# Kernel optimization log

Measured on AMD Instinct MI355X. Metric: run time of the kernel, lower is better.

## Reference

```python
import jax, jax.numpy as jnp
import numpy as np

N, C, D, H, W = 1, 32, 64, 192, 160


def affine_grid_3d(theta, size):
    # PyTorch F.affine_grid 3D, align_corners=True convention.
    n, c, d, h, w = size
    z = jnp.linspace(-1.0, 1.0, d)
    y = jnp.linspace(-1.0, 1.0, h)
    x = jnp.linspace(-1.0, 1.0, w)
    zz, yy, xx = jnp.meshgrid(z, y, x, indexing='ij')          # [D,H,W]
    base = jnp.stack([xx, yy, zz, jnp.ones_like(xx)], axis=-1)  # [D,H,W,4]
    return jnp.einsum('dhwk,nck->ndhwc', base, theta)           # [N,D,H,W,3] (x,y,z)


def _gather_corner(vol, zi, yi, xi):
    # vol: [C,D,H,W]; zi/yi/xi: [D,H,W] int32. Zero padding outside.
    c, d, h, w = vol.shape
    valid = (zi >= 0) & (zi < d) & (yi >= 0) & (yi < h) & (xi >= 0) & (xi < w)
    zc = jnp.clip(zi, 0, d - 1)
    yc = jnp.clip(yi, 0, h - 1)
    xc = jnp.clip(xi, 0, w - 1)
    flat = vol.reshape(c, d * h * w)
    idx = (zc * h + yc) * w + xc
    vals = jnp.take(flat, idx.reshape(-1), axis=1).reshape(c, *zi.shape)
    return vals * valid[None].astype(vol.dtype)


def grid_sample_3d(inp, grid):
    # Trilinear grid_sample, zeros padding, align_corners=True.
    n, c, d, h, w = inp.shape
    x = (grid[..., 0] + 1.0) * 0.5 * (w - 1)
    y = (grid[..., 1] + 1.0) * 0.5 * (h - 1)
    z = (grid[..., 2] + 1.0) * 0.5 * (d - 1)
    x0 = jnp.floor(x).astype(jnp.int32); x1 = x0 + 1
    y0 = jnp.floor(y).astype(jnp.int32); y1 = y0 + 1
    z0 = jnp.floor(z).astype(jnp.int32); z1 = z0 + 1
    wx = (x - x0.astype(x.dtype))
    wy = (y - y0.astype(y.dtype))
    wz = (z - z0.astype(z.dtype))

    def sample_one(vol, z0, z1, y0, y1, x0, x1, wz, wy, wx):
        out = jnp.zeros((vol.shape[0],) + wz.shape, dtype=vol.dtype)
        for zi, wzc in ((z0, 1.0 - wz), (z1, wz)):
            for yi, wyc in ((y0, 1.0 - wy), (y1, wy)):
                for xi, wxc in ((x0, 1.0 - wx), (x1, wx)):
                    out = out + _gather_corner(vol, zi, yi, xi) * (wzc * wyc * wxc)[None]
        return out

    return jax.vmap(sample_one)(inp, z0, z1, y0, y1, x0, x1, wz, wy, wx)


def setup_inputs() -> dict:
    key = jax.random.key(0)
    k1, k2 = jax.random.split(key)
    inp = jax.random.normal(k1, (N, C, D, H, W), dtype=jnp.float32)
    identity = jnp.asarray([1, 0, 0, 0, 0, 1, 0, 0, 0, 0, 1, 0], dtype=jnp.float32)
    theta = identity + 0.1 * jax.random.normal(k2, (12,), dtype=jnp.float32)
    return {"input": inp, "theta": theta}


def reference(input, theta):
    th = theta.reshape(1, 3, 4)
    grid = affine_grid_3d(th, input.shape)       # [N,D,H,W,3]
    out = grid_sample_3d(input, grid)            # [N,C,D,H,W]
    return jnp.transpose(out, (0, 4, 3, 1, 2))   # [N,W,H,C,D]
```

## Files before the change

### kernel.cpp

```cpp
#include <hip/hip_runtime.h>

constexpr int W_ = 160;
constexpr int H_ = 192;
constexpr int D_ = 64;
constexpr int C_ = 32;
constexpr int HW_  = H_ * W_;
constexpr int DHWi = D_ * HW_;
constexpr int CD   = C_ * D_;

constexpr int TW = 32, TH = 12, TD = 16;
constexpr int NWT = W_ / TW;
constexpr int NHT = H_ / TH;
constexpr int NDT = D_ / TD;
constexpr int QPP = NWT * NHT;
constexpr int CPX = C_ / 8;
constexpr int NPH = CPX * NDT;

typedef float f4_t __attribute__((ext_vector_type(4)));
typedef float f2_t __attribute__((ext_vector_type(2)));

__global__ void __launch_bounds__(256, 4)
affine_grid_sample_kernel(const float* __restrict__ inp,
                          const float* __restrict__ th,
                          float* __restrict__ out)
{
    const int t   = threadIdx.x;
    const int bid = blockIdx.x;
    const int xcd = bid & 7;
    int r = bid >> 3;
    const int phase = r / QPP;
    const int q     = r - phase * QPP;
    const int c  = xcd * CPX + (phase >> 2);
    const int dt = phase & 3;
    const int hs = q / NWT;
    const int wt = q - hs * NWT;
    const int w0 = wt * TW, h0 = hs * TH, d0 = dt * TD;

    const float th0=th[0], th1=th[1], th2 =th[2],  th3 =th[3];
    const float th4=th[4], th5=th[5], th6 =th[6],  th7 =th[7];
    const float th8=th[8], th9=th[9], th10=th[10], th11=th[11];

    const float* __restrict__ pc = inp + (size_t)c * DHWi;

    const int wl = t & 15;
    const int dq = (t >> 4) & 3;
    const int wh = (t >> 6) & 1;
    const int hp = t >> 7;
    const int w  = w0 + wh * 16 + wl;
    const float xx = fmaf((float)w, 2.0f / (W_ - 1), -1.0f);

    float kzx[4], kzy[4], kzz[4];
    #pragma unroll
    for (int k = 0; k < 4; ++k) {
        const int d = d0 + 4 * dq + k;
        const float zz = fmaf((float)d, 2.0f / (D_ - 1), -1.0f);
        kzx[k] = fmaf(th2,  zz, th3);
        kzy[k] = fmaf(th6,  zz, th7);
        kzz[k] = fmaf(th10, zz, th11);
    }

    float* const ob = out + ((size_t)w * H_ + h0) * CD + (size_t)c * D_ + d0 + 4 * dq;

    #pragma unroll 1
    for (int hh = hp; hh < TH; hh += 2) {
        const float yy = fmaf((float)(h0 + hh), 2.0f / (H_ - 1), -1.0f);

        unsigned off[4][4];
        float wA[4], wB[4], v0a[4], v1a[4], s0a[4], s1a[4];
        #pragma unroll
        for (int k = 0; k < 4; ++k) {
            const float px = (fmaf(th0, xx, fmaf(th1, yy, kzx[k])) + 1.0f) * (0.5f * (W_ - 1));
            const float py = (fmaf(th4, xx, fmaf(th5, yy, kzy[k])) + 1.0f) * (0.5f * (H_ - 1));
            const float pz = (fmaf(th8, xx, fmaf(th9, yy, kzz[k])) + 1.0f) * (0.5f * (D_ - 1));
            const float fx = floorf(px), fy = floorf(py), fz = floorf(pz);
            const int ix0 = (int)fx, iy0 = (int)fy, iz0 = (int)fz;
            const float wx = px - fx, wy = py - fy, wz = pz - fz;
            const float u0r = ((unsigned)ix0       < (unsigned)W_) ? (1.0f - wx) : 0.0f;
            const float u1r = ((unsigned)(ix0 + 1) < (unsigned)W_) ? wx          : 0.0f;
            v0a[k] = ((unsigned)iy0       < (unsigned)H_) ? (1.0f - wy) : 0.0f;
            v1a[k] = ((unsigned)(iy0 + 1) < (unsigned)H_) ? wy          : 0.0f;
            s0a[k] = ((unsigned)iz0       < (unsigned)D_) ? (1.0f - wz) : 0.0f;
            s1a[k] = ((unsigned)(iz0 + 1) < (unsigned)D_) ? wz          : 0.0f;
            float a = u0r, b = u1r;
            if (ix0 == -1)     { a = u1r; b = 0.0f; }
            if (ix0 == W_ - 1) { a = 0.0f; b = u0r; }
            wA[k] = a; wB[k] = b;
            const int e = min(max(ix0, 0), W_ - 2);
            const int cy0 = min(max(iy0,     0), H_ - 1);
            const int cy1 = min(max(iy0 + 1, 0), H_ - 1);
            const int cz0 = min(max(iz0,     0), D_ - 1);
            const int cz1 = min(max(iz0 + 1, 0), D_ - 1);
            off[k][0] = (unsigned)(cz0 * HW_ + cy0 * W_ + e);
            off[k][1] = (unsigned)(cz0 * HW_ + cy1 * W_ + e);
            off[k][2] = (unsigned)(cz1 * HW_ + cy0 * W_ + e);
            off[k][3] = (unsigned)(cz1 * HW_ + cy1 * W_ + e);
        }

        f2_t P[4][4];
        #pragma unroll
        for (int k = 0; k < 4; ++k)
            #pragma unroll
            for (int j = 0; j < 4; ++j)
                __builtin_memcpy(&P[k][j], pc + off[k][j], 8);

        asm volatile("" ::
            "v"(P[0][0]), "v"(P[0][1]), "v"(P[0][2]), "v"(P[0][3]),
            "v"(P[1][0]), "v"(P[1][1]), "v"(P[1][2]), "v"(P[1][3]),
            "v"(P[2][0]), "v"(P[2][1]), "v"(P[2][2]), "v"(P[2][3]),
            "v"(P[3][0]), "v"(P[3][1]), "v"(P[3][2]), "v"(P[3][3]));
        __builtin_amdgcn_sched_barrier(0);

        f4_t val;
        #pragma unroll
        for (int k = 0; k < 4; ++k) {
            const float x00 = wA[k] * P[k][0][0] + wB[k] * P[k][0][1];
            const float x01 = wA[k] * P[k][1][0] + wB[k] * P[k][1][1];
            const float x10 = wA[k] * P[k][2][0] + wB[k] * P[k][2][1];
            const float x11 = wA[k] * P[k][3][0] + wB[k] * P[k][3][1];
            const float e0 = v0a[k] * x00 + v1a[k] * x01;
            const float e1 = v0a[k] * x10 + v1a[k] * x11;
            val[k] = s0a[k] * e0 + s1a[k] * e1;
        }
        __builtin_nontemporal_store(val, (f4_t*)(ob + (size_t)hh * CD));
    }
}

extern "C" void kernel_launch(void* const* d_in, const int* in_sizes, int n_in,
                              void* d_out, int out_size, void* d_ws, size_t ws_size,
                              hipStream_t stream)
{
    const float* inp = (const float*)d_in[0];
    const float* th  = (const float*)d_in[1];
    float* out = (float*)d_out;

    hipLaunchKernelGGL(affine_grid_sample_kernel, dim3(8 * NPH * QPP), dim3(256),
                       0, stream, inp, th, out);
}
```

Baseline: 644.0 us.

## Stage sampled source bounding box in LDS before trilinear interpolation

```diff
diff --git a/kernel.cpp b/kernel.cpp
--- a/kernel.cpp
+++ b/kernel.cpp
@@ -8,13 +8,14 @@
 constexpr int DHWi = D_ * HW_;
 constexpr int CD   = C_ * D_;
 
-constexpr int TW = 32, TH = 12, TD = 16;
+constexpr int TW = 32, THh = 8, TDt = 4;
 constexpr int NWT = W_ / TW;
-constexpr int NHT = H_ / TH;
-constexpr int NDT = D_ / TD;
+constexpr int NHT = H_ / THh;
+constexpr int NDT = D_ / TDt;
 constexpr int QPP = NWT * NHT;
 constexpr int CPX = C_ / 8;
-constexpr int NPH = CPX * NDT;
+constexpr int BX = 44, BY = 24, BZ = 9;
+constexpr int TOT = BX * BY * BZ;
 
 typedef float f4_t __attribute__((ext_vector_type(4)));
 typedef float f2_t __attribute__((ext_vector_type(2)));
@@ -24,17 +25,19 @@
                           const float* __restrict__ th,
                           float* __restrict__ out)
 {
+    __shared__ float Lb[TOT];
+
     const int t   = threadIdx.x;
     const int bid = blockIdx.x;
     const int xcd = bid & 7;
-    int r = bid >> 3;
-    const int phase = r / QPP;
-    const int q     = r - phase * QPP;
-    const int c  = xcd * CPX + (phase >> 2);
-    const int dt = phase & 3;
-    const int hs = q / NWT;
-    const int wt = q - hs * NWT;
-    const int w0 = wt * TW, h0 = hs * TH, d0 = dt * TD;
+    const int r   = bid >> 3;
+    const int q   = r % QPP;
+    const int rem = r / QPP;
+    const int c   = xcd * CPX + (rem >> 4);
+    const int dt  = rem & 15;
+    const int hs  = q / NWT;
+    const int wt  = q - hs * NWT;
+    const int w0 = wt * TW, h0 = hs * THh, d0 = dt * TDt;
 
     const float th0=th[0], th1=th[1], th2 =th[2],  th3 =th[3];
     const float th4=th[4], th5=th[5], th6 =th[6],  th7 =th[7];
@@ -42,75 +45,179 @@
 
     const float* __restrict__ pc = inp + (size_t)c * DHWi;
 
-    const int wl = t & 15;
-    const int dq = (t >> 4) & 3;
-    const int wh = (t >> 6) & 1;
-    const int hp = t >> 7;
-    const int w  = w0 + wh * 16 + wl;
+    const int wl = t & 31;
+    const int hl = t >> 5;
+    const int w  = w0 + wl;
+    const int h  = h0 + hl;
     const float xx = fmaf((float)w, 2.0f / (W_ - 1), -1.0f);
-
-    float kzx[4], kzy[4], kzz[4];
+    const float yy = fmaf((float)h, 2.0f / (H_ - 1), -1.0f);
+
+    float pxmn= 1e30f, pxmx=-1e30f, pymn= 1e30f, pymx=-1e30f,
+          pzmn= 1e30f, pzmx=-1e30f;
+    #pragma unroll
+    for (int ci = 0; ci < 8; ++ci) {
+        const int cw = (ci & 1) ? w0 + TW  - 1 : w0;
+        const int chh= (ci & 2) ? h0 + THh - 1 : h0;
+        const int cd = (ci & 4) ? d0 + TDt - 1 : d0;
+        const float zzc = fmaf((float)cd, 2.0f / (D_ - 1), -1.0f);
+        const float kxc = fmaf(th2,  zzc, th3);
+        const float kyc = fmaf(th6,  zzc, th7);
+        const float kzc = fmaf(th10, zzc, th11);
+        const float xxc = fmaf((float)cw,  2.0f / (W_ - 1), -1.0f);
+        const float yyc = fmaf((float)chh, 2.0f / (H_ - 1), -1.0f);
+        const float px = (fmaf(th0, xxc, fmaf(th1, yyc, kxc)) + 1.0f) * (0.5f * (W_ - 1));
+        const float py = (fmaf(th4, xxc, fmaf(th5, yyc, kyc)) + 1.0f) * (0.5f * (H_ - 1));
+        const float pz = (fmaf(th8, xxc, fmaf(th9, yyc, kzc)) + 1.0f) * (0.5f * (D_ - 1));
+        pxmn = fminf(pxmn, px); pxmx = fmaxf(pxmx, px);
+        pymn = fminf(pymn, py); pymx = fmaxf(pymx, py);
+        pzmn = fminf(pzmn, pz); pzmx = fmaxf(pzmx, pz);
+    }
+    const int xlo = max((int)floorf(pxmn), 0);
+    const int xhi = min((int)floorf(pxmx) + 1, W_ - 1);
+    const int ylo = max((int)floorf(pymn), 0);
+    const int yhi = min((int)floorf(pymx) + 1, H_ - 1);
+    const int zlo = max((int)floorf(pzmn), 0);
+    const int zhi = min((int)floorf(pzmx) + 1, D_ - 1);
+    const bool fits = (xhi - xlo + 1 <= BX) && (yhi - ylo + 1 <= BY) &&
+                      (zhi - zlo + 1 <= BZ);
+
+    float wA[4], wB[4], v0a[4], v1a[4], s0a[4], s1a[4];
+    int   E[4], CY0[4], CY1[4], CZ0[4], CZ1[4];
     #pragma unroll
     for (int k = 0; k < 4; ++k) {
-        const int d = d0 + 4 * dq + k;
-        const float zz = fmaf((float)d, 2.0f / (D_ - 1), -1.0f);
-        kzx[k] = fmaf(th2,  zz, th3);
-        kzy[k] = fmaf(th6,  zz, th7);
-        kzz[k] = fmaf(th10, zz, th11);
+        const int d = d0 + k;
+        const float zz  = fmaf((float)d, 2.0f / (D_ - 1), -1.0f);
+        const float kzx = fmaf(th2,  zz, th3);
+        const float kzy = fmaf(th6,  zz, th7);
+        const float kzz = fmaf(th10, zz, th11);
+        const float px = (fmaf(th0, xx, fmaf(th1, yy, kzx)) + 1.0f) * (0.5f * (W_ - 1));
+        const float py = (fmaf(th4, xx, fmaf(th5, yy, kzy)) + 1.0f) * (0.5f * (H_ - 1));
+        const float pz = (fmaf(th8, xx, fmaf(th9, yy, kzz)) + 1.0f) * (0.5f * (D_ - 1));
+        const float fx = floorf(px), fy = floorf(py), fz = floorf(pz);
+        const int ix0 = (int)fx, iy0 = (int)fy, iz0 = (int)fz;
+        const float wx = px - fx, wy = py - fy, wz = pz - fz;
+        const float u0r = ((unsigned)ix0       < (unsigned)W_) ? (1.0f - wx) : 0.0f;
+        const float u1r = ((unsigned)(ix0 + 1) < (unsigned)W_) ? wx          : 0.0f;
+        v0a[k] = ((unsigned)iy0       < (unsigned)H_) ? (1.0f - wy) : 0.0f;
+        v1a[k] = ((unsigned)(iy0 + 1) < (unsigned)H_) ? wy          : 0.0f;
+        s0a[k] = ((unsigned)iz0       < (unsigned)D_) ? (1.0f - wz) : 0.0f;
+        s1a[k] = ((unsigned)(iz0 + 1) < (unsigned)D_) ? wz          : 0.0f;
+        float a = u0r, b = u1r;
+        if (ix0 == -1)     { a = u1r; b = 0.0f; }
+        if (ix0 == W_ - 1) { a = 0.0f; b = u0r; }
+        wA[k] = a; wB[k] = b;
+        E[k]   = min(max(ix0,     0), W_ - 2);
+        CY0[k] = min(max(iy0,     0), H_ - 1);
+        CY1[k] = min(max(iy0 + 1, 0), H_ - 1);
+        CZ0[k] = min(max(iz0,     0), D_ - 1);
+        CZ1[k] = min(max(iz0 + 1, 0), D_ - 1);
     }
 
-    float* const ob = out + ((size_t)w * H_ + h0) * CD + (size_t)c * D_ + d0 + 4 * dq;
-
-    #pragma unroll 1
-    for (int hh = hp; hh < TH; hh += 2) {
-        const float yy = fmaf((float)(h0 + hh), 2.0f / (H_ - 1), -1.0f);
-
-        unsigned off[4][4];
-        float wA[4], wB[4], v0a[4], v1a[4], s0a[4], s1a[4];
-        #pragma unroll
-        for (int k = 0; k < 4; ++k) {
-            const float px = (fmaf(th0, xx, fmaf(th1, yy, kzx[k])) + 1.0f) * (0.5f * (W_ - 1));
-            const float py = (fmaf(th4, xx, fmaf(th5, yy, kzy[k])) + 1.0f) * (0.5f * (H_ - 1));
-            const float pz = (fmaf(th8, xx, fmaf(th9, yy, kzz[k])) + 1.0f) * (0.5f * (D_ - 1));
-            const float fx = floorf(px), fy = floorf(py), fz = floorf(pz);
-            const int ix0 = (int)fx, iy0 = (int)fy, iz0 = (int)fz;
-            const float wx = px - fx, wy = py - fy, wz = pz - fz;
-            const float u0r = ((unsigned)ix0       < (unsigned)W_) ? (1.0f - wx) : 0.0f;
-            const float u1r = ((unsigned)(ix0 + 1) < (unsigned)W_) ? wx          : 0.0f;
-            v0a[k] = ((unsigned)iy0       < (unsigned)H_) ? (1.0f - wy) : 0.0f;
-            v1a[k] = ((unsigned)(iy0 + 1) < (unsigned)H_) ? wy          : 0.0f;
-            s0a[k] = ((unsigned)iz0       < (unsigned)D_) ? (1.0f - wz) : 0.0f;
-            s1a[k] = ((unsigned)(iz0 + 1) < (unsigned)D_) ? wz          : 0.0f;
-            float a = u0r, b = u1r;
-            if (ix0 == -1)     { a = u1r; b = 0.0f; }
-            if (ix0 == W_ - 1) { a = 0.0f; b = u0r; }
-            wA[k] = a; wB[k] = b;
-            const int e = min(max(ix0, 0), W_ - 2);
-            const int cy0 = min(max(iy0,     0), H_ - 1);
-            const int cy1 = min(max(iy0 + 1, 0), H_ - 1);
-            const int cz0 = min(max(iz0,     0), D_ - 1);
-            const int cz1 = min(max(iz0 + 1, 0), D_ - 1);
-            off[k][0] = (unsigned)(cz0 * HW_ + cy0 * W_ + e);
-            off[k][1] = (unsigned)(cz0 * HW_ + cy1 * W_ + e);
-            off[k][2] = (unsigned)(cz1 * HW_ + cy0 * W_ + e);
-            off[k][3] = (unsigned)(cz1 * HW_ + cy1 * W_ + e);
-        }
-
+    float* const ob = out + ((size_t)w * H_ + h) * CD + (size_t)c * D_ + d0;
+    f4_t val;
+
+    if (fits) {
+        const int wv = t >> 6, lane = t & 63;
+        const bool lx = (lane < BX);
+        const int gxl = min(xlo + lane, W_ - 1);
+        #pragma unroll
+        for (int rr = 0; rr < 4; ++rr) {
+            float v[12];
+            #pragma unroll
+            for (int bb = 0; bb < 2; ++bb) {
+                const int bz = 2 * rr + bb;
+                const int gz = min(zlo + bz, D_ - 1);
+                const float* __restrict__ rowz = pc + gz * HW_;
+                #pragma unroll
+                for (int i = 0; i < 6; ++i) {
+                    const int gy = min(ylo + wv + i * 4, H_ - 1);
+                    v[bb * 6 + i] = lx ? rowz[gy * W_ + gxl] : 0.0f;
+                }
+            }
+            asm volatile("" :: "v"(v[0]), "v"(v[1]), "v"(v[2]),  "v"(v[3]),
+                               "v"(v[4]), "v"(v[5]), "v"(v[6]),  "v"(v[7]),
+                               "v"(v[8]), "v"(v[9]), "v"(v[10]), "v"(v[11]));
+            #pragma unroll
+            for (int bb = 0; bb < 2; ++bb) {
+                const int bz = 2 * rr + bb;
+                #pragma unroll
+                for (int i = 0; i < 6; ++i) {
+                    const int by = wv + i * 4;
+                    if (lx) Lb[(bz * BY + by) * BX + lane] = v[bb * 6 + i];
+                }
+            }
+        }
+        {
+            const int gz = min(zlo + 8, D_ - 1);
+            const float* __restrict__ rowz = pc + gz * HW_;
+            float v[6];
+            #pragma unroll
+            for (int i = 0; i < 6; ++i) {
+                const int gy = min(ylo + wv + i * 4, H_ - 1);
+                v[i] = lx ? rowz[gy * W_ + gxl] : 0.0f;
+            }
+            asm volatile("" :: "v"(v[0]), "v"(v[1]), "v"(v[2]),
+                               "v"(v[3]), "v"(v[4]), "v"(v[5]));
+            #pragma unroll
+            for (int i = 0; i < 6; ++i) {
+                const int by = wv + i * 4;
+                if (lx) Lb[(8 * BY + by) * BX + lane] = v[i];
+            }
+        }
+        __syncthreads();
+
+        float p0[4][4], p1[4][4];
+        #pragma unroll
+        for (int k = 0; k < 4; ++k) {
+            const int rx  = E[k] - xlo;
+            const int r00 = ((CZ0[k] - zlo) * BY + (CY0[k] - ylo)) * BX + rx;
+            const int r01 = ((CZ0[k] - zlo) * BY + (CY1[k] - ylo)) * BX + rx;
+            const int r10 = ((CZ1[k] - zlo) * BY + (CY0[k] - ylo)) * BX + rx;
+            const int r11 = ((CZ1[k] - zlo) * BY + (CY1[k] - ylo)) * BX + rx;
+            p0[k][0] = Lb[r00]; p1[k][0] = Lb[r00 + 1];
+            p0[k][1] = Lb[r01]; p1[k][1] = Lb[r01 + 1];
+            p0[k][2] = Lb[r10]; p1[k][2] = Lb[r10 + 1];
+            p0[k][3] = Lb[r11]; p1[k][3] = Lb[r11 + 1];
+        }
+        asm volatile("" ::
+            "v"(p0[0][0]), "v"(p0[0][1]), "v"(p0[0][2]), "v"(p0[0][3]),
+            "v"(p0[1][0]), "v"(p0[1][1]), "v"(p0[1][2]), "v"(p0[1][3]),
+            "v"(p0[2][0]), "v"(p0[2][1]), "v"(p0[2][2]), "v"(p0[2][3]),
+            "v"(p0[3][0]), "v"(p0[3][1]), "v"(p0[3][2]), "v"(p0[3][3]),
+            "v"(p1[0][0]), "v"(p1[0][1]), "v"(p1[0][2]), "v"(p1[0][3]),
+            "v"(p1[1][0]), "v"(p1[1][1]), "v"(p1[1][2]), "v"(p1[1][3]),
+            "v"(p1[2][0]), "v"(p1[2][1]), "v"(p1[2][2]), "v"(p1[2][3]),
+            "v"(p1[3][0]), "v"(p1[3][1]), "v"(p1[3][2]), "v"(p1[3][3]));
+        __builtin_amdgcn_sched_barrier(0);
+        #pragma unroll
+        for (int k = 0; k < 4; ++k) {
+            const float x00 = wA[k] * p0[k][0] + wB[k] * p1[k][0];
+            const float x01 = wA[k] * p0[k][1] + wB[k] * p1[k][1];
+            const float x10 = wA[k] * p0[k][2] + wB[k] * p1[k][2];
+            const float x11 = wA[k] * p0[k][3] + wB[k] * p1[k][3];
+            const float e0 = v0a[k] * x00 + v1a[k] * x01;
+            const float e1 = v0a[k] * x10 + v1a[k] * x11;
+            val[k] = s0a[k] * e0 + s1a[k] * e1;
+        }
+    } else {
         f2_t P[4][4];
         #pragma unroll
-        for (int k = 0; k < 4; ++k)
-            #pragma unroll
-            for (int j = 0; j < 4; ++j)
-                __builtin_memcpy(&P[k][j], pc + off[k][j], 8);
-
+        for (int k = 0; k < 4; ++k) {
+            const unsigned o0 = (unsigned)(CZ0[k] * HW_ + CY0[k] * W_ + E[k]);
+            const unsigned o1 = (unsigned)(CZ0[k] * HW_ + CY1[k] * W_ + E[k]);
+            const unsigned o2 = (unsigned)(CZ1[k] * HW_ + CY0[k] * W_ + E[k]);
+            const unsigned o3 = (unsigned)(CZ1[k] * HW_ + CY1[k] * W_ + E[k]);
+            __builtin_memcpy(&P[k][0], pc + o0, 8);
+            __builtin_memcpy(&P[k][1], pc + o1, 8);
+            __builtin_memcpy(&P[k][2], pc + o2, 8);
+            __builtin_memcpy(&P[k][3], pc + o3, 8);
+        }
         asm volatile("" ::
             "v"(P[0][0]), "v"(P[0][1]), "v"(P[0][2]), "v"(P[0][3]),
             "v"(P[1][0]), "v"(P[1][1]), "v"(P[1][2]), "v"(P[1][3]),
             "v"(P[2][0]), "v"(P[2][1]), "v"(P[2][2]), "v"(P[2][3]),
             "v"(P[3][0]), "v"(P[3][1]), "v"(P[3][2]), "v"(P[3][3]));
         __builtin_amdgcn_sched_barrier(0);
-
-        f4_t val;
         #pragma unroll
         for (int k = 0; k < 4; ++k) {
             const float x00 = wA[k] * P[k][0][0] + wB[k] * P[k][0][1];
@@ -121,8 +228,9 @@
             const float e1 = v0a[k] * x10 + v1a[k] * x11;
             val[k] = s0a[k] * e0 + s1a[k] * e1;
         }
-        __builtin_nontemporal_store(val, (f4_t*)(ob + (size_t)hh * CD));
     }
+
+    __builtin_nontemporal_store(val, (f4_t*)ob);
 }
 
 extern "C" void kernel_launch(void* const* d_in, const int* in_sizes, int n_in,
@@ -133,6 +241,6 @@
     const float* th  = (const float*)d_in[1];
     float* out = (float*)d_out;
 
-    hipLaunchKernelGGL(affine_grid_sample_kernel, dim3(8 * NPH * QPP), dim3(256),
-                       0, stream, inp, th, out);
+    hipLaunchKernelGGL(affine_grid_sample_kernel, dim3(8 * CPX * NDT * QPP),
+                       dim3(256), 0, stream, inp, th, out);
 }
```

Result: slower. 1.060 ms (+64.6%).

## Stage source bounding box into LDS via global_load_lds before trilinear gather

Applied to the files above, without the earlier changes.

```diff
diff --git a/kernel.cpp b/kernel.cpp
--- a/kernel.cpp
+++ b/kernel.cpp
@@ -8,13 +8,15 @@
 constexpr int DHWi = D_ * HW_;
 constexpr int CD   = C_ * D_;
 
-constexpr int TW = 32, TH = 12, TD = 16;
+constexpr int TW = 16, TH = 8, TD = 16;
 constexpr int NWT = W_ / TW;
 constexpr int NHT = H_ / TH;
 constexpr int NDT = D_ / TD;
 constexpr int QPP = NWT * NHT;
 constexpr int CPX = C_ / 8;
-constexpr int NPH = CPX * NDT;
+constexpr int BXF   = 32;
+constexpr int RMAX  = 420;
+constexpr int LROWS = RMAX + 2;
 
 typedef float f4_t __attribute__((ext_vector_type(4)));
 typedef float f2_t __attribute__((ext_vector_type(2)));
@@ -24,16 +26,18 @@
                           const float* __restrict__ th,
                           float* __restrict__ out)
 {
+    __shared__ float Lb[BXF * LROWS];
+
     const int t   = threadIdx.x;
     const int bid = blockIdx.x;
     const int xcd = bid & 7;
-    int r = bid >> 3;
-    const int phase = r / QPP;
-    const int q     = r - phase * QPP;
-    const int c  = xcd * CPX + (phase >> 2);
-    const int dt = phase & 3;
-    const int hs = q / NWT;
-    const int wt = q - hs * NWT;
+    const int r_  = bid >> 3;
+    const int q   = r_ % QPP;
+    const int rem = r_ / QPP;
+    const int c   = xcd * CPX + (rem >> 2);
+    const int dt  = rem & 3;
+    const int hs  = q / NWT;
+    const int wt  = q - hs * NWT;
     const int w0 = wt * TW, h0 = hs * TH, d0 = dt * TD;
 
     const float th0=th[0], th1=th[1], th2 =th[2],  th3 =th[3];
@@ -42,87 +46,141 @@
 
     const float* __restrict__ pc = inp + (size_t)c * DHWi;
 
-    const int wl = t & 15;
-    const int dq = (t >> 4) & 3;
-    const int wh = (t >> 6) & 1;
-    const int hp = t >> 7;
-    const int w  = w0 + wh * 16 + wl;
+    float pxmn= 1e30f, pxmx=-1e30f, pymn= 1e30f, pymx=-1e30f,
+          pzmn= 1e30f, pzmx=-1e30f;
+    #pragma unroll
+    for (int ci = 0; ci < 8; ++ci) {
+        const int cw = (ci & 1) ? w0 + TW - 1 : w0;
+        const int chh= (ci & 2) ? h0 + TH - 1 : h0;
+        const int cd = (ci & 4) ? d0 + TD - 1 : d0;
+        const float zzc = fmaf((float)cd, 2.0f / (D_ - 1), -1.0f);
+        const float kxc = fmaf(th2,  zzc, th3);
+        const float kyc = fmaf(th6,  zzc, th7);
+        const float kzc = fmaf(th10, zzc, th11);
+        const float xxc = fmaf((float)cw,  2.0f / (W_ - 1), -1.0f);
+        const float yyc = fmaf((float)chh, 2.0f / (H_ - 1), -1.0f);
+        const float px = (fmaf(th0, xxc, fmaf(th1, yyc, kxc)) + 1.0f) * (0.5f * (W_ - 1));
+        const float py = (fmaf(th4, xxc, fmaf(th5, yyc, kyc)) + 1.0f) * (0.5f * (H_ - 1));
+        const float pz = (fmaf(th8, xxc, fmaf(th9, yyc, kzc)) + 1.0f) * (0.5f * (D_ - 1));
+        pxmn = fminf(pxmn, px); pxmx = fmaxf(pxmx, px);
+        pymn = fminf(pymn, py); pymx = fmaxf(pymx, py);
+        pzmn = fminf(pzmn, pz); pzmx = fmaxf(pzmx, pz);
+    }
+    const int xlo = max((int)floorf(pxmn), 0);
+    const int xhi = min((int)floorf(pxmx) + 1, W_ - 1);
+    const int ylo = max((int)floorf(pymn), 0);
+    const int yhi = min((int)floorf(pymx) + 1, H_ - 1);
+    const int zlo = max((int)floorf(pzmn), 0);
+    const int zhi = min((int)floorf(pzmx) + 1, D_ - 1);
+    const int BXr = xhi - xlo + 1;
+    const int BYr = yhi - ylo + 1;
+    const int BZr = zhi - zlo + 1;
+    const int R   = BZr * BYr;
+    const bool fits = (BXr <= BXF) && (BYr <= 128) && (R <= RMAX);
+
+    if (fits) {
+        const int lane = t & 63, wv = t >> 6;
+        const int half = lane >> 5;
+        const int lx   = lane & 31;
+        const unsigned m18 = (262144u + (unsigned)BYr - 1) / (unsigned)BYr;
+        const int npair = (R + 1) >> 1;
+        for (int p = wv; p < npair; p += 4) {
+            const int rr = 2 * p + half;
+            const int bz = (int)(((unsigned)rr * m18) >> 18);
+            const int by = rr - bz * BYr;
+            const int gz = min(zlo + bz, D_ - 1);
+            const int gy = min(ylo + by, H_ - 1);
+            const int gx = min(xlo + lx, W_ - 1);
+            const float* gsrc = pc + ((unsigned)(gz * HW_ + gy * W_ + gx));
+            __builtin_amdgcn_global_load_lds(
+                (const __attribute__((address_space(1))) unsigned*)gsrc,
+                (__attribute__((address_space(3))) unsigned*)&Lb[(2 * p) * BXF],
+                4, 0, 0);
+        }
+        asm volatile("s_waitcnt vmcnt(0)" ::: "memory");
+    }
+    __syncthreads();
+
+    const int dq = t & 1;
+    const int wl = (t >> 1) & 15;
+    const int hl = t >> 5;
+    const int w  = w0 + wl;
+    const int h  = h0 + hl;
     const float xx = fmaf((float)w, 2.0f / (W_ - 1), -1.0f);
+    const float yy = fmaf((float)h, 2.0f / (H_ - 1), -1.0f);
 
-    float kzx[4], kzy[4], kzz[4];
+    f4_t val0, val1;
     #pragma unroll
-    for (int k = 0; k < 4; ++k) {
-        const int d = d0 + 4 * dq + k;
-        const float zz = fmaf((float)d, 2.0f / (D_ - 1), -1.0f);
-        kzx[k] = fmaf(th2,  zz, th3);
-        kzy[k] = fmaf(th6,  zz, th7);
-        kzz[k] = fmaf(th10, zz, th11);
+    for (int k = 0; k < 8; ++k) {
+        const int d = d0 + (k & 3) + dq * 4 + (k >> 2) * 8;
+        const float zz  = fmaf((float)d, 2.0f / (D_ - 1), -1.0f);
+        const float kzx = fmaf(th2,  zz, th3);
+        const float kzy = fmaf(th6,  zz, th7);
+        const float kzz = fmaf(th10, zz, th11);
+        const float px = (fmaf(th0, xx, fmaf(th1, yy, kzx)) + 1.0f) * (0.5f * (W_ - 1));
+        const float py = (fmaf(th4, xx, fmaf(th5, yy, kzy)) + 1.0f) * (0.5f * (H_ - 1));
+        const float pz = (fmaf(th8, xx, fmaf(th9, yy, kzz)) + 1.0f) * (0.5f * (D_ - 1));
+        const float fx = floorf(px), fy = floorf(py), fz = floorf(pz);
+        const int ix0 = (int)fx, iy0 = (int)fy, iz0 = (int)fz;
+        const float wx = px - fx, wy = py - fy, wz = pz - fz;
+        const float u0r = ((unsigned)ix0       < (unsigned)W_) ? (1.0f - wx) : 0.0f;
+        const float u1r = ((unsigned)(ix0 + 1) < (unsigned)W_) ? wx          : 0.0f;
+        const float v0  = ((unsigned)iy0       < (unsigned)H_) ? (1.0f - wy) : 0.0f;
+        const float v1  = ((unsigned)(iy0 + 1) < (unsigned)H_) ? wy          : 0.0f;
+        const float s0  = ((unsigned)iz0       < (unsigned)D_) ? (1.0f - wz) : 0.0f;
+        const float s1  = ((unsigned)(iz0 + 1) < (unsigned)D_) ? wz          : 0.0f;
+        float wA = u0r, wB = u1r;
+        if (ix0 == -1)     { wA = u1r; wB = 0.0f; }
+        if (ix0 == W_ - 1) { wA = 0.0f; wB = u0r; }
+        const int e   = min(max(ix0,     0), W_ - 2);
+        const int cy0 = min(max(iy0,     0), H_ - 1);
+        const int cy1 = min(max(iy0 + 1, 0), H_ - 1);
+        const int cz0 = min(max(iz0,     0), D_ - 1);
+        const int cz1 = min(max(iz0 + 1, 0), D_ - 1);
+
+        float a00, b00, a01, b01, a10, b10, a11, b11;
+        if (__builtin_expect(fits, 1)) {
+            const int bx  = e - xlo;
+            const int r00 = (cz0 - zlo) * BYr + (cy0 - ylo);
+            const int r01 = (cz0 - zlo) * BYr + (cy1 - ylo);
+            const int r10 = (cz1 - zlo) * BYr + (cy0 - ylo);
+            const int r11 = (cz1 - zlo) * BYr + (cy1 - ylo);
+            const float* L00 = &Lb[(r00 << 5) + bx];
+            const float* L01 = &Lb[(r01 << 5) + bx];
+            const float* L10 = &Lb[(r10 << 5) + bx];
+            const float* L11 = &Lb[(r11 << 5) + bx];
+            a00 = L00[0]; b00 = L00[1];
+            a01 = L01[0]; b01 = L01[1];
+            a10 = L10[0]; b10 = L10[1];
+            a11 = L11[0]; b11 = L11[1];
+        } else {
+            f2_t P0, P1, P2, P3;
+            const unsigned o0 = (unsigned)(cz0 * HW_ + cy0 * W_ + e);
+            const unsigned o1 = (unsigned)(cz0 * HW_ + cy1 * W_ + e);
+            const unsigned o2 = (unsigned)(cz1 * HW_ + cy0 * W_ + e);
+            const unsigned o3 = (unsigned)(cz1 * HW_ + cy1 * W_ + e);
+            __builtin_memcpy(&P0, pc + o0, 8);
+            __builtin_memcpy(&P1, pc + o1, 8);
+            __builtin_memcpy(&P2, pc + o2, 8);
+            __builtin_memcpy(&P3, pc + o3, 8);
+            asm volatile("" :: "v"(P0), "v"(P1), "v"(P2), "v"(P3));
+            a00 = P0[0]; b00 = P0[1]; a01 = P1[0]; b01 = P1[1];
+            a10 = P2[0]; b10 = P2[1]; a11 = P3[0]; b11 = P3[1];
+        }
+
+        const float x00 = wA * a00 + wB * b00;
+        const float x01 = wA * a01 + wB * b01;
+        const float x10 = wA * a10 + wB * b10;
+        const float x11 = wA * a11 + wB * b11;
+        const float e0 = v0 * x00 + v1 * x01;
+        const float e1 = v0 * x10 + v1 * x11;
+        const float v  = s0 * e0 + s1 * e1;
+        if (k < 4) val0[k] = v; else val1[k - 4] = v;
     }
 
-    float* const ob = out + ((size_t)w * H_ + h0) * CD + (size_t)c * D_ + d0 + 4 * dq;
-
-    #pragma unroll 1
-    for (int hh = hp; hh < TH; hh += 2) {
-        const float yy = fmaf((float)(h0 + hh), 2.0f / (H_ - 1), -1.0f);
-
-        unsigned off[4][4];
-        float wA[4], wB[4], v0a[4], v1a[4], s0a[4], s1a[4];
-        #pragma unroll
-        for (int k = 0; k < 4; ++k) {
-            const float px = (fmaf(th0, xx, fmaf(th1, yy, kzx[k])) + 1.0f) * (0.5f * (W_ - 1));
-            const float py = (fmaf(th4, xx, fmaf(th5, yy, kzy[k])) + 1.0f) * (0.5f * (H_ - 1));
-            const float pz = (fmaf(th8, xx, fmaf(th9, yy, kzz[k])) + 1.0f) * (0.5f * (D_ - 1));
-            const float fx = floorf(px), fy = floorf(py), fz = floorf(pz);
-            const int ix0 = (int)fx, iy0 = (int)fy, iz0 = (int)fz;
-            const float wx = px - fx, wy = py - fy, wz = pz - fz;
-            const float u0r = ((unsigned)ix0       < (unsigned)W_) ? (1.0f - wx) : 0.0f;
-            const float u1r = ((unsigned)(ix0 + 1) < (unsigned)W_) ? wx          : 0.0f;
-            v0a[k] = ((unsigned)iy0       < (unsigned)H_) ? (1.0f - wy) : 0.0f;
-            v1a[k] = ((unsigned)(iy0 + 1) < (unsigned)H_) ? wy          : 0.0f;
-            s0a[k] = ((unsigned)iz0       < (unsigned)D_) ? (1.0f - wz) : 0.0f;
-            s1a[k] = ((unsigned)(iz0 + 1) < (unsigned)D_) ? wz          : 0.0f;
-            float a = u0r, b = u1r;
-            if (ix0 == -1)     { a = u1r; b = 0.0f; }
-            if (ix0 == W_ - 1) { a = 0.0f; b = u0r; }
-            wA[k] = a; wB[k] = b;
-            const int e = min(max(ix0, 0), W_ - 2);
-            const int cy0 = min(max(iy0,     0), H_ - 1);
-            const int cy1 = min(max(iy0 + 1, 0), H_ - 1);
-            const int cz0 = min(max(iz0,     0), D_ - 1);
-            const int cz1 = min(max(iz0 + 1, 0), D_ - 1);
-            off[k][0] = (unsigned)(cz0 * HW_ + cy0 * W_ + e);
-            off[k][1] = (unsigned)(cz0 * HW_ + cy1 * W_ + e);
-            off[k][2] = (unsigned)(cz1 * HW_ + cy0 * W_ + e);
-            off[k][3] = (unsigned)(cz1 * HW_ + cy1 * W_ + e);
-        }
-
-        f2_t P[4][4];
-        #pragma unroll
-        for (int k = 0; k < 4; ++k)
-            #pragma unroll
-            for (int j = 0; j < 4; ++j)
-                __builtin_memcpy(&P[k][j], pc + off[k][j], 8);
-
-        asm volatile("" ::
-            "v"(P[0][0]), "v"(P[0][1]), "v"(P[0][2]), "v"(P[0][3]),
-            "v"(P[1][0]), "v"(P[1][1]), "v"(P[1][2]), "v"(P[1][3]),
-            "v"(P[2][0]), "v"(P[2][1]), "v"(P[2][2]), "v"(P[2][3]),
-            "v"(P[3][0]), "v"(P[3][1]), "v"(P[3][2]), "v"(P[3][3]));
-        __builtin_amdgcn_sched_barrier(0);
-
-        f4_t val;
-        #pragma unroll
-        for (int k = 0; k < 4; ++k) {
-            const float x00 = wA[k] * P[k][0][0] + wB[k] * P[k][0][1];
-            const float x01 = wA[k] * P[k][1][0] + wB[k] * P[k][1][1];
-            const float x10 = wA[k] * P[k][2][0] + wB[k] * P[k][2][1];
-            const float x11 = wA[k] * P[k][3][0] + wB[k] * P[k][3][1];
-            const float e0 = v0a[k] * x00 + v1a[k] * x01;
-            const float e1 = v0a[k] * x10 + v1a[k] * x11;
-            val[k] = s0a[k] * e0 + s1a[k] * e1;
-        }
-        __builtin_nontemporal_store(val, (f4_t*)(ob + (size_t)hh * CD));
-    }
+    float* const ob = out + ((size_t)w * H_ + h) * CD + (size_t)c * D_ + d0 + dq * 4;
+    __builtin_nontemporal_store(val0, (f4_t*)ob);
+    __builtin_nontemporal_store(val1, (f4_t*)(ob + 8));
 }
 
 extern "C" void kernel_launch(void* const* d_in, const int* in_sizes, int n_in,
@@ -133,6 +191,6 @@
     const float* th  = (const float*)d_in[1];
     float* out = (float*)d_out;
 
-    hipLaunchKernelGGL(affine_grid_sample_kernel, dim3(8 * NPH * QPP), dim3(256),
-                       0, stream, inp, th, out);
+    hipLaunchKernelGGL(affine_grid_sample_kernel, dim3(8 * CPX * NDT * QPP),
+                       dim3(256), 0, stream, inp, th, out);
 }
```

Measured after the change: 640.1 us. No clear change (-0.6%).
